# Kernel tuning notes

Measured on AMD Instinct MI355X. Metric: run time of the kernel, lower is better.

## Reference

```python
import jax, jax.numpy as jnp
import numpy as np

B, S, D, H, M = 4, 4096, 768, 12, 256
Dh = D // H
EPS_KERNEL = 1e-4
LN_EPS = 1e-5


def setup_inputs() -> dict:
    key = jax.random.key(0)
    ks = jax.random.split(key, 18)
    w = lambda k, sh: jax.random.normal(k, sh, jnp.float32) * 0.02
    return {
        "x": jax.random.normal(ks[0], (B, S, D), jnp.float32),
        # FAVOR+ random projection (performer uses orthogonal gaussian; gaussian here, same math)
        "proj": jax.random.normal(ks[1], (M, Dh), jnp.float32),
        "wq": w(ks[2], (D, D)), "bq": jnp.zeros((D,), jnp.float32),
        "wk": w(ks[3], (D, D)), "bk": jnp.zeros((D,), jnp.float32),
        "wv": w(ks[4], (D, D)), "bv": jnp.zeros((D,), jnp.float32),
        "wo": w(ks[5], (D, D)), "bo": jnp.zeros((D,), jnp.float32),
        "ln1_g": jnp.ones((D,), jnp.float32), "ln1_b": jnp.zeros((D,), jnp.float32),
        "ln2_g": jnp.ones((D,), jnp.float32), "ln2_b": jnp.zeros((D,), jnp.float32),
        "w1": w(ks[6], (4 * D, D)), "b1": jnp.zeros((4 * D,), jnp.float32),
        "w2": w(ks[7], (D, 4 * D)), "b2": jnp.zeros((D,), jnp.float32),
    }


def layernorm(x, g, b):
    mu = x.mean(-1, keepdims=True)
    var = ((x - mu) ** 2).mean(-1, keepdims=True)
    return (x - mu) / jnp.sqrt(var + LN_EPS) * g + b


def softmax_features(data, proj, is_query):
    # FAVOR+ positive softmax kernel features (performer-pytorch softmax_kernel)
    norm = data.shape[-1] ** -0.25
    ratio = proj.shape[0] ** -0.5
    dd = jnp.einsum('bhnd,md->bhnm', data * norm, proj)       # [B,H,S,M]
    diag = (data ** 2).sum(-1, keepdims=True) * 0.5 * norm * norm
    if is_query:
        mx = jnp.max(dd, axis=-1, keepdims=True)
    else:
        mx = jnp.max(dd)
    return ratio * (jnp.exp(dd - diag - mx) + EPS_KERNEL)


def performer_block(x, proj, wq, bq, wk, bk, wv, bv, wo, bo,
                    ln1_g, ln1_b, ln2_g, ln2_b, w1, b1, w2, b2):
    h = layernorm(x, ln1_g, ln1_b)
    split = lambda t: t.reshape(B, S, H, Dh).transpose(0, 2, 1, 3)  # [B,H,S,Dh]
    q = split(h @ wq.T + bq)
    k = split(h @ wk.T + bk)
    v = split(h @ wv.T + bv)

    qp = softmax_features(q, proj, True)    # [B,H,S,M]
    kp = softmax_features(k, proj, False)   # [B,H,S,M]

    # non-causal linear attention
    k_sum = kp.sum(axis=2)                                   # [B,H,M]
    d_inv = 1.0 / jnp.einsum('bhnm,bhm->bhn', qp, k_sum)     # [B,H,S]
    ctx = jnp.einsum('bhnm,bhnd->bhmd', kp, v)               # [B,H,M,Dh]
    attn = jnp.einsum('bhnm,bhmd,bhn->bhnd', qp, ctx, d_inv) # [B,H,S,Dh]
    attn = attn.transpose(0, 2, 1, 3).reshape(B, S, D)
    x = x + attn @ wo.T + bo

    h2 = layernorm(x, ln2_g, ln2_b)
    h2 = jax.nn.gelu(h2 @ w1.T + b1, approximate=False)
    x = x + h2 @ w2.T + b2
    return x


def reference(x, proj, wq, bq, wk, bk, wv, bv, wo, bo,
              ln1_g, ln1_b, ln2_g, ln2_b, w1, b1, w2, b2):
    return performer_block(x, proj, wq, bq, wk, bk, wv, bv, wo, bo,
                           ln1_g, ln1_b, ln2_g, ln2_b, w1, b1, w2, b2)
```

## Files before the change

kernel.cpp:

```cpp
#include <hip/hip_runtime.h>
#include <math.h>

typedef __attribute__((ext_vector_type(8))) short bf16x8;
typedef __attribute__((ext_vector_type(4))) float f32x4;

__device__ __forceinline__ float b2f(unsigned short u) {
    return __uint_as_float(((unsigned)u) << 16);
}
__device__ __forceinline__ unsigned short f2b(float f) {
    unsigned u = __float_as_uint(f);
    u += 0x7FFF + ((u >> 16) & 1);
    return (unsigned short)(u >> 16);
}
__device__ __forceinline__ void up2(unsigned u, float& a, float& b) {
    a = __uint_as_float(u << 16);
    b = __uint_as_float(u & 0xffff0000u);
}
__device__ __forceinline__ float gelu_exact(float v) {
    return 0.5f * v * (1.0f + erff(v * 0.70710678118654752f));
}
__device__ __forceinline__ void atomicMaxFloat(float* addr, float val) {
    unsigned* ua = (unsigned*)addr;
    unsigned old = *ua;
    while (true) {
        float of = __uint_as_float(old);
        if (of >= val) break;
        unsigned assumed = old;
        old = atomicCAS(ua, assumed, __float_as_uint(val));
        if (old == assumed) break;
    }
}
__device__ __forceinline__ void gl_lds16(const unsigned short* g, unsigned short* lds) {
    __builtin_amdgcn_global_load_lds((const __attribute__((address_space(1))) unsigned int*)g,
                                     (__attribute__((address_space(3))) unsigned int*)lds, 16, 0, 0);
}

__global__ void init_kernel(float* ksum, float* kmax) {
    int i = blockIdx.x * 256 + threadIdx.x;
    if (i < 48 * 256) ksum[i] = 0.0f;
    if (i == 0) *kmax = -3.0e38f;
}

__global__ __launch_bounds__(256)
void cvt_qkvp(const float* __restrict__ wq, const float* __restrict__ wk, const float* __restrict__ wv,
              const float* __restrict__ prj, unsigned short* __restrict__ wdst,
              unsigned short* __restrict__ pdst) {
    int i4 = (blockIdx.x * 256 + threadIdx.x) * 4;
    const float* s; unsigned short* d; int off;
    if (i4 < 1769472) { s = (i4 < 589824) ? wq : (i4 < 1179648 ? wk : wv);
        off = (i4 < 589824) ? i4 : (i4 < 1179648 ? i4 - 589824 : i4 - 1179648);
        d = wdst + i4; }
    else { s = prj; off = i4 - 1769472; d = pdst + off; }
    float4 v = *(const float4*)&s[off];
    ushort4 o; o.x = f2b(v.x); o.y = f2b(v.y); o.z = f2b(v.z); o.w = f2b(v.w);
    *(ushort4*)d = o;
}
__global__ __launch_bounds__(256)
void cvt_ow12(const float* __restrict__ wo, const float* __restrict__ w1, const float* __restrict__ w2,
              unsigned short* __restrict__ dst) {
    int i4 = (blockIdx.x * 256 + threadIdx.x) * 4;
    const float* s; int off;
    if (i4 < 589824) { s = wo; off = i4; }
    else if (i4 < 2949120) { s = w1; off = i4 - 589824; }
    else { s = w2; off = i4 - 2949120; }
    float4 v = *(const float4*)&s[off];
    ushort4 o; o.x = f2b(v.x); o.y = f2b(v.y); o.z = f2b(v.z); o.w = f2b(v.w);
    *(ushort4*)&dst[i4] = o;
}

template <bool IN_F32>
__global__ __launch_bounds__(256)
void ln_kernel(const void* __restrict__ Xv, const float* __restrict__ G,
               const float* __restrict__ Bb, unsigned short* __restrict__ OUT) {
    int row = blockIdx.x, t = threadIdx.x, wave = t >> 6, lane = t & 63;
    __shared__ float red[4];
    float x0, x1, x2;
    if constexpr (IN_F32) {
        const float* xr = (const float*)Xv + (size_t)row * 768;
        x0 = xr[t]; x1 = xr[t + 256]; x2 = xr[t + 512];
    } else {
        const unsigned short* xr = (const unsigned short*)Xv + (size_t)row * 768;
        x0 = b2f(xr[t]); x1 = b2f(xr[t + 256]); x2 = b2f(xr[t + 512]);
    }
    float s = x0 + x1 + x2;
#pragma unroll
    for (int d = 32; d; d >>= 1) s += __shfl_xor(s, d, 64);
    if (lane == 0) red[wave] = s;
    __syncthreads();
    float mean = (red[0] + red[1] + red[2] + red[3]) * (1.0f / 768.0f);
    __syncthreads();
    float d0 = x0 - mean, d1 = x1 - mean, d2 = x2 - mean;
    float s2 = d0 * d0 + d1 * d1 + d2 * d2;
#pragma unroll
    for (int d = 32; d; d >>= 1) s2 += __shfl_xor(s2, d, 64);
    if (lane == 0) red[wave] = s2;
    __syncthreads();
    float var = (red[0] + red[1] + red[2] + red[3]) * (1.0f / 768.0f);
    float inv = rsqrtf(var + 1e-5f);
    size_t base = (size_t)row * 768;
    OUT[base + t]       = f2b(d0 * inv * G[t]       + Bb[t]);
    OUT[base + t + 256] = f2b(d1 * inv * G[t + 256] + Bb[t + 256]);
    OUT[base + t + 512] = f2b(d2 * inv * G[t + 512] + Bb[t + 512]);
}

template <int EPI, bool R_F32, bool C_F32>
__global__ __launch_bounds__(256)
void gemm_bt_128(const unsigned short* __restrict__ A, const unsigned short* __restrict__ Bm,
                 const float* __restrict__ bias, const void* __restrict__ R,
                 void* __restrict__ C, int N, int K, float alpha) {
    __shared__ unsigned short sA[2][128 * 32];
    __shared__ unsigned short sB[2][128 * 32];
    const int t = threadIdx.x;
    const int wave = t >> 6, lane = t & 63, quad = lane >> 4, l16 = lane & 15;
    const int m0 = blockIdx.y * 128, n0 = blockIdx.x * 128;
    const int wm = (wave >> 1) * 64, wn = (wave & 1) * 64;
    const int srow = t >> 2;
    const int scol = ((t & 3) ^ (srow & 3)) << 3;
    const unsigned short* ga0 = &A[(size_t)(m0 + srow) * K + scol];
    const unsigned short* ga1 = &A[(size_t)(m0 + 64 + srow) * K + scol];
    const unsigned short* gb0 = &Bm[(size_t)(n0 + srow) * K + scol];
    const unsigned short* gb1 = &Bm[(size_t)(n0 + 64 + srow) * K + scol];
    const int ldsoff = wave * 512;
    int raoff[4], rboff[4];
#pragma unroll
    for (int i = 0; i < 4; ++i) {
        const int sw = ((quad ^ l16) & 3) << 3;
        raoff[i] = (wm + i * 16 + l16) * 32 + sw;
        rboff[i] = (wn + i * 16 + l16) * 32 + sw;
    }
    f32x4 acc[4][4] = {};
    const int nt = K >> 5;
    gl_lds16(ga0, &sA[0][ldsoff]);
    gl_lds16(ga1, &sA[0][2048 + ldsoff]);
    gl_lds16(gb0, &sB[0][ldsoff]);
    gl_lds16(gb1, &sB[0][2048 + ldsoff]);
    __syncthreads();
    int cur = 0;
    for (int it = 0; it < nt; ++it) {
        if (it + 1 < nt) {
            const int kt = (it + 1) << 5;
            gl_lds16(ga0 + kt, &sA[cur ^ 1][ldsoff]);
            gl_lds16(ga1 + kt, &sA[cur ^ 1][2048 + ldsoff]);
            gl_lds16(gb0 + kt, &sB[cur ^ 1][ldsoff]);
            gl_lds16(gb1 + kt, &sB[cur ^ 1][2048 + ldsoff]);
        }
        bf16x8 af[4], bfr[4];
#pragma unroll
        for (int i = 0; i < 4; ++i) af[i] = *(const bf16x8*)&sA[cur][raoff[i]];
#pragma unroll
        for (int j = 0; j < 4; ++j) bfr[j] = *(const bf16x8*)&sB[cur][rboff[j]];
#pragma unroll
        for (int i = 0; i < 4; ++i)
#pragma unroll
            for (int j = 0; j < 4; ++j)
                acc[i][j] = __builtin_amdgcn_mfma_f32_16x16x32_bf16(af[i], bfr[j], acc[i][j], 0, 0, 0);
        __syncthreads();
        cur ^= 1;
    }
    if constexpr (EPI == 3) {
#pragma unroll
        for (int i = 0; i < 4; ++i) {
            int rowb = m0 + wm + i * 16 + quad * 4;
            int b_ = rowb >> 12, sbase = rowb & 4095;
#pragma unroll
            for (int j = 0; j < 4; ++j) {
                int col = n0 + wn + j * 16 + l16;
                float bs = bias[col];
                ushort4 o;
                o.x = f2b(acc[i][j][0] + bs);
                o.y = f2b(acc[i][j][1] + bs);
                o.z = f2b(acc[i][j][2] + bs);
                o.w = f2b(acc[i][j][3] + bs);
                size_t dst = (((size_t)b_ * 12 + (col >> 6)) * 64 + (col & 63)) * 4096 + sbase;
                *(ushort4*)&((unsigned short*)C)[dst] = o;
            }
        }
        return;
    }
#pragma unroll
    for (int i = 0; i < 4; ++i) {
        int rowb = m0 + wm + i * 16 + quad * 4;
#pragma unroll
        for (int j = 0; j < 4; ++j) {
            int col = n0 + wn + j * 16 + l16;
            float bs = bias[col];
#pragma unroll
            for (int r = 0; r < 4; ++r) {
                size_t idx = (size_t)(rowb + r) * N + col;
                float v = acc[i][j][r] + bs;
                if constexpr (EPI == 0) v *= alpha;
                if constexpr (EPI == 1) {
                    if constexpr (R_F32) v += ((const float*)R)[idx];
                    else                 v += b2f(((const unsigned short*)R)[idx]);
                }
                if constexpr (EPI == 2) v = gelu_exact(v);
                if constexpr (C_F32) ((float*)C)[idx] = v;
                else                 ((unsigned short*)C)[idx] = f2b(v);
            }
        }
    }
}

template <int MODE>
__global__ __launch_bounds__(256)
void feat_kernel(const unsigned short* __restrict__ Q, const unsigned short* __restrict__ P,
                 unsigned short* __restrict__ OUTP, float* __restrict__ kmaxp,
                 float* __restrict__ ksump) {
    __shared__ unsigned short sQ[64 * 64];
    __shared__ unsigned short sP[256 * 64];
    __shared__ float sDiag[64];
    __shared__ float sRed[4];
    int t = threadIdx.x, wave = t >> 6, lane = t & 63, quad = lane >> 4, l16 = lane & 15;
    int bh = blockIdx.y, bq = bh / 12, hh = bh % 12;
    int s0 = blockIdx.x * 64;
    size_t rowbase = (size_t)bq * 4096 + s0;
#pragma unroll
    for (int u = 0; u < 2; ++u) {
        int L = u * 256 + t, row = L >> 3, c8 = (L & 7) * 8;
        *(uint4*)&sQ[row * 64 + c8] = *(const uint4*)&Q[(rowbase + row) * 768 + hh * 64 + c8];
    }
#pragma unroll
    for (int u = 0; u < 8; ++u) {
        int L = u * 256 + t, row = L >> 3, c8 = (L & 7) * 8;
        *(uint4*)&sP[row * 64 + c8] = *(const uint4*)&P[(size_t)row * 64 + c8];
    }
    __syncthreads();
    if (MODE != 1 && t < 64) {
        float d = 0.0f;
        for (int c = 0; c < 64; ++c) { float f = b2f(sQ[t * 64 + c]); d += f * f; }
        sDiag[t] = 0.5f * d;
    }
    f32x4 acc[4][4] = {};
#pragma unroll
    for (int ks = 0; ks < 2; ++ks) {
        bf16x8 af[4], bfr[4];
#pragma unroll
        for (int i = 0; i < 4; ++i) af[i] = *(const bf16x8*)&sQ[(i * 16 + l16) * 64 + ks * 32 + quad * 8];
#pragma unroll
        for (int j = 0; j < 4; ++j) bfr[j] = *(const bf16x8*)&sP[(wave * 64 + j * 16 + l16) * 64 + ks * 32 + quad * 8];
#pragma unroll
        for (int i = 0; i < 4; ++i)
#pragma unroll
            for (int j = 0; j < 4; ++j)
                acc[i][j] = __builtin_amdgcn_mfma_f32_16x16x32_bf16(af[i], bfr[j], acc[i][j], 0, 0, 0);
    }
    if constexpr (MODE == 1) {
        float m = -3.0e38f;
#pragma unroll
        for (int i = 0; i < 4; ++i)
#pragma unroll
            for (int j = 0; j < 4; ++j)
#pragma unroll
                for (int r = 0; r < 4; ++r) m = fmaxf(m, acc[i][j][r]);
#pragma unroll
        for (int d = 1; d < 64; d <<= 1) m = fmaxf(m, __shfl_xor(m, d, 64));
        if (lane == 0) sRed[wave] = m;
        __syncthreads();
        if (t == 0) atomicMaxFloat(kmaxp, fmaxf(fmaxf(sRed[0], sRed[1]), fmaxf(sRed[2], sRed[3])));
        return;
    } else {
        __syncthreads();
        float mx_k = *kmaxp;
        float csum[4] = {0.0f, 0.0f, 0.0f, 0.0f};
#pragma unroll
        for (int i = 0; i < 4; ++i)
#pragma unroll
            for (int j = 0; j < 4; ++j) {
                int col = wave * 64 + j * 16 + l16;
                ushort4 o;
#pragma unroll
                for (int r = 0; r < 4; ++r) {
                    int row = i * 16 + quad * 4 + r;
                    float v = 0.0625f * (expf(acc[i][j][r] - sDiag[row] - mx_k) + 1e-4f);
                    csum[j] += v;
                    (&o.x)[r] = f2b(v);
                }
                *(ushort4*)&OUTP[((size_t)bh * 256 + col) * 4096 + s0 + i * 16 + quad * 4] = o;
            }
#pragma unroll
        for (int j = 0; j < 4; ++j) {
            csum[j] += __shfl_xor(csum[j], 16, 64);
            csum[j] += __shfl_xor(csum[j], 32, 64);
        }
        if (quad == 0)
#pragma unroll
            for (int j = 0; j < 4; ++j)
                atomicAdd(&ksump[bh * 256 + wave * 64 + j * 16 + l16], csum[j]);
    }
}

__global__ __launch_bounds__(256)
void ctx_gemm(const unsigned short* __restrict__ KPT, const unsigned short* __restrict__ VT,
              float* __restrict__ part) {
    __shared__ unsigned short sV[2][64 * 32];
    __shared__ unsigned short sK[2][128 * 32];
    const int t = threadIdx.x;
    const int wave = t >> 6, lane = t & 63, quad = lane >> 4, l16 = lane & 15;
    const int bh = blockIdx.y;
    const int sc = blockIdx.x >> 1, mh = blockIdx.x & 1;
    const int m0 = mh * 128;
    const int k0 = sc * 512;
    const int srow = t >> 2;
    const int scol = ((t & 3) ^ (srow & 3)) << 3;
    const unsigned short* gv  = &VT [((size_t)bh * 64 + srow) * 4096 + k0 + scol];
    const unsigned short* gk0 = &KPT[((size_t)bh * 256 + m0 + srow) * 4096 + k0 + scol];
    const unsigned short* gk1 = &KPT[((size_t)bh * 256 + m0 + 64 + srow) * 4096 + k0 + scol];
    const int ldsoff = wave * 512;
    const int sw = ((quad ^ l16) & 3) << 3;
    f32x4 acc[4][2] = {};
    gl_lds16(gv,  &sV[0][ldsoff]);
    gl_lds16(gk0, &sK[0][ldsoff]);
    gl_lds16(gk1, &sK[0][2048 + ldsoff]);
    __syncthreads();
    int cur = 0;
    for (int it = 0; it < 16; ++it) {
        if (it + 1 < 16) {
            const int kt = (it + 1) << 5;
            gl_lds16(gv + kt,  &sV[cur ^ 1][ldsoff]);
            gl_lds16(gk0 + kt, &sK[cur ^ 1][ldsoff]);
            gl_lds16(gk1 + kt, &sK[cur ^ 1][2048 + ldsoff]);
        }
        bf16x8 af[4], bfr[2];
#pragma unroll
        for (int i = 0; i < 4; ++i) af[i] = *(const bf16x8*)&sV[cur][(i * 16 + l16) * 32 + sw];
#pragma unroll
        for (int j = 0; j < 2; ++j) bfr[j] = *(const bf16x8*)&sK[cur][(wave * 32 + j * 16 + l16) * 32 + sw];
#pragma unroll
        for (int i = 0; i < 4; ++i)
#pragma unroll
            for (int j = 0; j < 2; ++j)
                acc[i][j] = __builtin_amdgcn_mfma_f32_16x16x32_bf16(af[i], bfr[j], acc[i][j], 0, 0, 0);
        __syncthreads();
        cur ^= 1;
    }
    float* base = part + ((size_t)(sc * 48 + bh) * 64) * 256;
#pragma unroll
    for (int i = 0; i < 4; ++i)
#pragma unroll
        for (int r = 0; r < 4; ++r) {
            int d = i * 16 + quad * 4 + r;
#pragma unroll
            for (int j = 0; j < 2; ++j) {
                int m = m0 + wave * 32 + j * 16 + l16;
                base[(size_t)d * 256 + m] = acc[i][j][r];
            }
        }
}

__global__ __launch_bounds__(256)
void ctx_reduce(const float* __restrict__ part, unsigned short* __restrict__ ctxb) {
    size_t i = (size_t)blockIdx.x * 256 + threadIdx.x;
    float s = 0.0f;
#pragma unroll
    for (int c = 0; c < 8; ++c) s += part[(size_t)c * 786432 + i];
    ctxb[i] = f2b(s);
}

__global__ __launch_bounds__(256)
void feat_attn(const unsigned short* __restrict__ Q, const unsigned short* __restrict__ P,
               const unsigned short* __restrict__ CTX, const float* __restrict__ ksump,
               unsigned short* __restrict__ ATT) {
    __shared__ unsigned short sQ[64 * 64];
    __shared__ unsigned short sPQ[256 * 64];
    __shared__ unsigned short sCtx[64 * 256];
    __shared__ float sDiag[64];
    __shared__ float sRed[256];
    __shared__ float sWred[256];
    __shared__ float sKs[256];
    __shared__ float sDinv[64];
    int t = threadIdx.x, wave = t >> 6, lane = t & 63, quad = lane >> 4, l16 = lane & 15;
    int bh = blockIdx.y, bq = bh / 12, hh = bh % 12;
    int s0 = blockIdx.x * 64;
    size_t rowbase = (size_t)bq * 4096 + s0;
#pragma unroll
    for (int u = 0; u < 2; ++u) {
        int L = u * 256 + t, row = L >> 3, c8 = (L & 7) * 8;
        *(uint4*)&sQ[row * 64 + c8] = *(const uint4*)&Q[(rowbase + row) * 768 + hh * 64 + c8];
    }
#pragma unroll
    for (int u = 0; u < 8; ++u) {
        int L = u * 256 + t, row = L >> 3, c8 = (L & 7) * 8;
        *(uint4*)&sPQ[row * 64 + c8] = *(const uint4*)&P[(size_t)row * 64 + c8];
    }
#pragma unroll
    for (int u = 0; u < 8; ++u) {
        int L = u * 256 + t, d = L >> 5, m8 = L & 31;
        int m8s = (m8 & 28) | ((m8 ^ d) & 3);
        *(uint4*)&sCtx[d * 256 + m8s * 8] = *(const uint4*)&CTX[(size_t)bh * 16384 + d * 256 + m8 * 8];
    }
    sKs[t] = ksump[bh * 256 + t];
    __syncthreads();
    if (t < 64) {
        float d = 0.0f;
        for (int c = 0; c < 64; ++c) { float f = b2f(sQ[t * 64 + c]); d += f * f; }
        sDiag[t] = 0.5f * d;
    }
    f32x4 acc[4][4] = {};
#pragma unroll
    for (int ks = 0; ks < 2; ++ks) {
        bf16x8 af[4], bfr[4];
#pragma unroll
        for (int i = 0; i < 4; ++i) af[i] = *(const bf16x8*)&sQ[(i * 16 + l16) * 64 + ks * 32 + quad * 8];
#pragma unroll
        for (int j = 0; j < 4; ++j) bfr[j] = *(const bf16x8*)&sPQ[(wave * 64 + j * 16 + l16) * 64 + ks * 32 + quad * 8];
#pragma unroll
        for (int i = 0; i < 4; ++i)
#pragma unroll
            for (int j = 0; j < 4; ++j)
                acc[i][j] = __builtin_amdgcn_mfma_f32_16x16x32_bf16(af[i], bfr[j], acc[i][j], 0, 0, 0);
    }
#pragma unroll
    for (int i = 0; i < 4; ++i)
#pragma unroll
        for (int r = 0; r < 4; ++r) {
            float m = fmaxf(fmaxf(acc[i][0][r], acc[i][1][r]), fmaxf(acc[i][2][r], acc[i][3][r]));
#pragma unroll
            for (int d = 1; d < 16; d <<= 1) m = fmaxf(m, __shfl_xor(m, d, 64));
            if (l16 == 0) sRed[wave * 64 + i * 16 + quad * 4 + r] = m;
        }
    __syncthreads();
    if (t < 64) sRed[t] = fmaxf(fmaxf(sRed[t], sRed[64 + t]), fmaxf(sRed[128 + t], sRed[192 + t]));
    __syncthreads();
#pragma unroll
    for (int i = 0; i < 4; ++i)
#pragma unroll
        for (int r = 0; r < 4; ++r) {
            int row = i * 16 + quad * 4 + r;
            float diag = sDiag[row], mx = sRed[row];
            float p = 0.0f;
#pragma unroll
            for (int j = 0; j < 4; ++j) {
                int col = wave * 64 + j * 16 + l16;
                float v = 0.0625f * (expf(acc[i][j][r] - diag - mx) + 1e-4f);
                int colp = (col & ~31) | ((((col >> 3) ^ row) & 3) << 3) | (col & 7);
                sPQ[row * 256 + colp] = f2b(v);
                p += v * sKs[col];
            }
#pragma unroll
            for (int d = 1; d < 16; d <<= 1) p += __shfl_xor(p, d, 64);
            if (l16 == 0) sWred[wave * 64 + row] = p;
        }
    __syncthreads();
    if (t < 64) sDinv[t] = 1.0f / (sWred[t] + sWred[64 + t] + sWred[128 + t] + sWred[192 + t]);
    __syncthreads();
    const int w16 = wave * 16;
    const int aswz = ((quad ^ (l16 & 3)) << 3);
    f32x4 acc2[4] = {};
    const unsigned short* qrow = &sPQ[(w16 + l16) * 256];
#pragma unroll
    for (int kt = 0; kt < 256; kt += 32) {
        bf16x8 af = *(const bf16x8*)&qrow[kt + aswz];
#pragma unroll
        for (int j = 0; j < 4; ++j) {
            bf16x8 bf = *(const bf16x8*)&sCtx[(j * 16 + l16) * 256 + kt + aswz];
            acc2[j] = __builtin_amdgcn_mfma_f32_16x16x32_bf16(af, bf, acc2[j], 0, 0, 0);
        }
    }
#pragma unroll
    for (int rr = 0; rr < 4; ++rr) {
        int sr = w16 + quad * 4 + rr;
        float dv = sDinv[sr];
        size_t obase = ((size_t)bq * 4096 + s0 + sr) * 768 + hh * 64;
#pragma unroll
        for (int j = 0; j < 4; ++j)
            ATT[obase + j * 16 + l16] = f2b(acc2[j][rr] * dv);
    }
}

extern "C" void kernel_launch(void* const* d_in, const int* in_sizes, int n_in,
                              void* d_out, int out_size, void* d_ws, size_t ws_size,
                              hipStream_t stream) {
    const float* X   = (const float*)d_in[0];
    const float* PRJ = (const float*)d_in[1];
    const float* WQ  = (const float*)d_in[2];
    const float* BQ  = (const float*)d_in[3];
    const float* WK  = (const float*)d_in[4];
    const float* BKb = (const float*)d_in[5];
    const float* WV  = (const float*)d_in[6];
    const float* BV  = (const float*)d_in[7];
    const float* WO  = (const float*)d_in[8];
    const float* BO  = (const float*)d_in[9];
    const float* G1  = (const float*)d_in[10];
    const float* Bn1 = (const float*)d_in[11];
    const float* G2  = (const float*)d_in[12];
    const float* Bn2 = (const float*)d_in[13];
    const float* W1  = (const float*)d_in[14];
    const float* Bf1 = (const float*)d_in[15];
    const float* W2  = (const float*)d_in[16];
    const float* Bf2 = (const float*)d_in[17];
    float* OUT = (float*)d_out;

    char* w = (char*)d_ws;
    const size_t SZ_ACT = (size_t)16384 * 768 * 2;
    unsigned short* hbuf  = (unsigned short*)(w);
    float*          part  = (float*)(w);
    unsigned short* qn    = (unsigned short*)(w + SZ_ACT);
    unsigned short* wow12 = (unsigned short*)(w + SZ_ACT);
    unsigned short* kn    = (unsigned short*)(w + 2 * SZ_ACT);
    unsigned short* x2    = (unsigned short*)(w + 2 * SZ_ACT);
    unsigned short* vtb   = (unsigned short*)(w + 3 * SZ_ACT);
    unsigned short* attn  = (unsigned short*)(w + 3 * SZ_ACT);
    unsigned short* wqkv  = (unsigned short*)(w + 4 * SZ_ACT);
    unsigned short* kpt   = (unsigned short*)(w + 4 * SZ_ACT);
    unsigned short* gmid  = kpt;
    char* tail = w + 4 * SZ_ACT + (size_t)100663296;
    unsigned short* prjb = (unsigned short*)(tail);
    unsigned short* ctxb = (unsigned short*)(tail + 32768);
    float* ksum = (float*)(tail + 32768 + 1572864);
    float* kmax = (float*)(tail + 32768 + 1572864 + 49152);

    unsigned short* wqb = wqkv;
    unsigned short* wkb = wqkv + 589824;
    unsigned short* wvb = wqkv + 1179648;
    unsigned short* wob = wow12;
    unsigned short* w1b = wow12 + 589824;
    unsigned short* w2b = wow12 + 2949120;

    const float NORM = 0.35355339059327373f;

    init_kernel<<<48, 256, 0, stream>>>(ksum, kmax);
    cvt_qkvp<<<1744, 256, 0, stream>>>(WQ, WK, WV, PRJ, wqkv, prjb);
    ln_kernel<true><<<16384, 256, 0, stream>>>(X, G1, Bn1, hbuf);
    gemm_bt_128<0, false, false><<<dim3(6, 128), 256, 0, stream>>>(hbuf, wqb, BQ, nullptr, qn, 768, 768, NORM);
    gemm_bt_128<0, false, false><<<dim3(6, 128), 256, 0, stream>>>(hbuf, wkb, BKb, nullptr, kn, 768, 768, NORM);
    gemm_bt_128<3, false, false><<<dim3(6, 128), 256, 0, stream>>>(hbuf, wvb, BV, nullptr, vtb, 768, 768, 1.0f);
    feat_kernel<1><<<dim3(64, 48), 256, 0, stream>>>(kn, prjb, nullptr, kmax, ksum);
    feat_kernel<2><<<dim3(64, 48), 256, 0, stream>>>(kn, prjb, kpt, kmax, ksum);
    ctx_gemm<<<dim3(16, 48), 256, 0, stream>>>(kpt, vtb, part);
    ctx_reduce<<<3072, 256, 0, stream>>>(part, ctxb);
    feat_attn<<<dim3(64, 48), 256, 0, stream>>>(qn, prjb, ctxb, ksum, attn);
    cvt_ow12<<<5184, 256, 0, stream>>>(WO, W1, W2, wow12);
    gemm_bt_128<1, true, false><<<dim3(6, 128), 256, 0, stream>>>(attn, wob, BO, X, x2, 768, 768, 1.0f);
    ln_kernel<false><<<16384, 256, 0, stream>>>(x2, G2, Bn2, hbuf);
    gemm_bt_128<2, false, false><<<dim3(24, 128), 256, 0, stream>>>(hbuf, w1b, Bf1, nullptr, gmid, 3072, 768, 1.0f);
    gemm_bt_128<1, false, true><<<dim3(6, 128), 256, 0, stream>>>(gmid, w2b, Bf2, x2, OUT, 768, 3072, 1.0f);
}
```

Measured before the change: 803.0 us.

## Enlarge GEMM tile to 256x128 with 8 waves and XCD-aware block swizzle

Grows the bf16 MFMA GEMM block tile from 128x128 to 256x128, using 512 threads (8 waves) that share one B tile in LDS. This halves the B-tile loads per output element and halves the block count. It also remaps the flat block index so neighbouring tiles land on the same XCD, aiming for better L2 reuse. The larger tile raises LDS use and block size, which may lower occupancy and leave fewer blocks to fill the CUs on the smaller GEMMs.

```diff
diff --git a/kernel.cpp b/kernel.cpp
--- a/kernel.cpp
+++ b/kernel.cpp
@@ -104,45 +104,48 @@
 }
 
 template <int EPI, bool R_F32, bool C_F32>
-__global__ __launch_bounds__(256)
-void gemm_bt_128(const unsigned short* __restrict__ A, const unsigned short* __restrict__ Bm,
+__global__ __launch_bounds__(512)
+void gemm_bt_256(const unsigned short* __restrict__ A, const unsigned short* __restrict__ Bm,
                  const float* __restrict__ bias, const void* __restrict__ R,
                  void* __restrict__ C, int N, int K, float alpha) {
-    __shared__ unsigned short sA[2][128 * 32];
+    __shared__ unsigned short sA[2][256 * 32];
     __shared__ unsigned short sB[2][128 * 32];
     const int t = threadIdx.x;
     const int wave = t >> 6, lane = t & 63, quad = lane >> 4, l16 = lane & 15;
-    const int m0 = blockIdx.y * 128, n0 = blockIdx.x * 128;
+    const int nwg = gridDim.x * gridDim.y;
+    int flat = blockIdx.y * gridDim.x + blockIdx.x;
+    int q = nwg >> 3, r = nwg & 7;
+    int xcd = flat & 7, idx = flat >> 3;
+    int swz = (xcd < r ? xcd * (q + 1) : r * (q + 1) + (xcd - r) * q) + idx;
+    const int m0 = (swz / gridDim.x) * 256;
+    const int n0 = (swz % gridDim.x) * 128;
     const int wm = (wave >> 1) * 64, wn = (wave & 1) * 64;
     const int srow = t >> 2;
     const int scol = ((t & 3) ^ (srow & 3)) << 3;
     const unsigned short* ga0 = &A[(size_t)(m0 + srow) * K + scol];
-    const unsigned short* ga1 = &A[(size_t)(m0 + 64 + srow) * K + scol];
-    const unsigned short* gb0 = &Bm[(size_t)(n0 + srow) * K + scol];
-    const unsigned short* gb1 = &Bm[(size_t)(n0 + 64 + srow) * K + scol];
+    const unsigned short* ga1 = &A[(size_t)(m0 + 128 + srow) * K + scol];
+    const unsigned short* gb  = &Bm[(size_t)(n0 + srow) * K + scol];
     const int ldsoff = wave * 512;
+    const int sw = ((quad ^ l16) & 3) << 3;
     int raoff[4], rboff[4];
 #pragma unroll
     for (int i = 0; i < 4; ++i) {
-        const int sw = ((quad ^ l16) & 3) << 3;
         raoff[i] = (wm + i * 16 + l16) * 32 + sw;
         rboff[i] = (wn + i * 16 + l16) * 32 + sw;
     }
     f32x4 acc[4][4] = {};
     const int nt = K >> 5;
     gl_lds16(ga0, &sA[0][ldsoff]);
-    gl_lds16(ga1, &sA[0][2048 + ldsoff]);
-    gl_lds16(gb0, &sB[0][ldsoff]);
-    gl_lds16(gb1, &sB[0][2048 + ldsoff]);
+    gl_lds16(ga1, &sA[0][4096 + ldsoff]);
+    gl_lds16(gb,  &sB[0][ldsoff]);
     __syncthreads();
     int cur = 0;
     for (int it = 0; it < nt; ++it) {
         if (it + 1 < nt) {
             const int kt = (it + 1) << 5;
             gl_lds16(ga0 + kt, &sA[cur ^ 1][ldsoff]);
-            gl_lds16(ga1 + kt, &sA[cur ^ 1][2048 + ldsoff]);
-            gl_lds16(gb0 + kt, &sB[cur ^ 1][ldsoff]);
-            gl_lds16(gb1 + kt, &sB[cur ^ 1][2048 + ldsoff]);
+            gl_lds16(ga1 + kt, &sA[cur ^ 1][4096 + ldsoff]);
+            gl_lds16(gb + kt,  &sB[cur ^ 1][ldsoff]);
         }
         bf16x8 af[4], bfr[4];
 #pragma unroll
@@ -185,9 +188,9 @@
             int col = n0 + wn + j * 16 + l16;
             float bs = bias[col];
 #pragma unroll
-            for (int r = 0; r < 4; ++r) {
-                size_t idx = (size_t)(rowb + r) * N + col;
-                float v = acc[i][j][r] + bs;
+            for (int r4 = 0; r4 < 4; ++r4) {
+                size_t idx = (size_t)(rowb + r4) * N + col;
+                float v = acc[i][j][r4] + bs;
                 if constexpr (EPI == 0) v *= alpha;
                 if constexpr (EPI == 1) {
                     if constexpr (R_F32) v += ((const float*)R)[idx];
@@ -521,17 +524,17 @@
     init_kernel<<<48, 256, 0, stream>>>(ksum, kmax);
     cvt_qkvp<<<1744, 256, 0, stream>>>(WQ, WK, WV, PRJ, wqkv, prjb);
     ln_kernel<true><<<16384, 256, 0, stream>>>(X, G1, Bn1, hbuf);
-    gemm_bt_128<0, false, false><<<dim3(6, 128), 256, 0, stream>>>(hbuf, wqb, BQ, nullptr, qn, 768, 768, NORM);
-    gemm_bt_128<0, false, false><<<dim3(6, 128), 256, 0, stream>>>(hbuf, wkb, BKb, nullptr, kn, 768, 768, NORM);
-    gemm_bt_128<3, false, false><<<dim3(6, 128), 256, 0, stream>>>(hbuf, wvb, BV, nullptr, vtb, 768, 768, 1.0f);
+    gemm_bt_256<0, false, false><<<dim3(6, 64), 512, 0, stream>>>(hbuf, wqb, BQ, nullptr, qn, 768, 768, NORM);
+    gemm_bt_256<0, false, false><<<dim3(6, 64), 512, 0, stream>>>(hbuf, wkb, BKb, nullptr, kn, 768, 768, NORM);
+    gemm_bt_256<3, false, false><<<dim3(6, 64), 512, 0, stream>>>(hbuf, wvb, BV, nullptr, vtb, 768, 768, 1.0f);
     feat_kernel<1><<<dim3(64, 48), 256, 0, stream>>>(kn, prjb, nullptr, kmax, ksum);
     feat_kernel<2><<<dim3(64, 48), 256, 0, stream>>>(kn, prjb, kpt, kmax, ksum);
     ctx_gemm<<<dim3(16, 48), 256, 0, stream>>>(kpt, vtb, part);
     ctx_reduce<<<3072, 256, 0, stream>>>(part, ctxb);
     feat_attn<<<dim3(64, 48), 256, 0, stream>>>(qn, prjb, ctxb, ksum, attn);
     cvt_ow12<<<5184, 256, 0, stream>>>(WO, W1, W2, wow12);
-    gemm_bt_128<1, true, false><<<dim3(6, 128), 256, 0, stream>>>(attn, wob, BO, X, x2, 768, 768, 1.0f);
+    gemm_bt_256<1, true, false><<<dim3(6, 64), 512, 0, stream>>>(attn, wob, BO, X, x2, 768, 768, 1.0f);
     ln_kernel<false><<<16384, 256, 0, stream>>>(x2, G2, Bn2, hbuf);
-    gemm_bt_128<2, false, false><<<dim3(24, 128), 256, 0, stream>>>(hbuf, w1b, Bf1, nullptr, gmid, 3072, 768, 1.0f);
-    gemm_bt_128<1, false, true><<<dim3(6, 128), 256, 0, stream>>>(gmid, w2b, Bf2, x2, OUT, 768, 3072, 1.0f);
-}
+    gemm_bt_256<2, false, false><<<dim3(24, 64), 512, 0, stream>>>(hbuf, w1b, Bf1, nullptr, gmid, 3072, 768, 1.0f);
+    gemm_bt_256<1, false, true><<<dim3(6, 64), 512, 0, stream>>>(gmid, w2b, Bf2, x2, OUT, 768, 3072, 1.0f);
+}
```

Result: no change. 811.8 us (+1.1%).
